# Performance work log

Hardware: AMD Instinct MI355X
Metric: run time of the kernel (lower is better)

The kernel has to match this reference:

```python
import jax, jax.numpy as jnp
import numpy as np

# normalization module stand-ins (simple monotone scalings, as in the repo they
# are fixed elementwise rescalings of the raw quantities)
def norm_local_x(n):
    return n

def norm_unit_contraction(c):
    return c

def norm_local_N(N):
    return jnp.log1p(N.astype(jnp.float32))

norm_TNG_radii = norm_local_x
norm_local_v = norm_local_x
norm_local_v0 = norm_local_x

EPS = 1e-5


def setup_inputs() -> dict:
    key = jax.random.key(0)
    ks = jax.random.split(key, 12)
    B, T, ND, KB = 2, 1024, 256, 3
    K_IN, H, L = 19, 128, 128
    x0 = 0.3 * jax.random.normal(ks[0], (B, T, 3), dtype=jnp.float32)
    # DM positions in local frame, |x| must stay < 1.05 (assert in original)
    x = jax.random.uniform(ks[1], (B, T, ND, 3), dtype=jnp.float32) - 0.5
    N = jax.random.randint(ks[2], (B, T), 1, 512, dtype=jnp.int32)
    basis = jax.random.normal(ks[3], (B, KB, 3), dtype=jnp.float32)
    v = jax.random.normal(ks[4], (B, T, ND, 3), dtype=jnp.float32)
    P200c = 0.5 + jax.random.uniform(ks[5], (B,), dtype=jnp.float32)
    s = 0.1
    W0 = s * jax.random.normal(ks[6], (K_IN, H - 1), dtype=jnp.float32)
    b0 = jnp.zeros((H - 1,), jnp.float32)
    W1 = s * jax.random.normal(ks[7], (H, H), dtype=jnp.float32)
    b1 = jnp.zeros((H,), jnp.float32)
    W2 = s * jax.random.normal(ks[8], (H, L), dtype=jnp.float32)
    b2 = jnp.zeros((L,), jnp.float32)
    return {"x0": x0, "x": x, "N": N, "basis": basis, "v": v, "P200c": P200c,
            "W0": W0, "b0": b0, "W1": W1, "b1": b1, "W2": W2, "b2": b2}


def create_scalars(x0, x, N, basis, v):
    B, T, ND, _ = x.shape
    # velocities relative to local mean (halo -> local frame)
    v0 = jnp.mean(v, axis=2)                      # [B,T,3]
    vc = v - v0[:, :, None, :]                    # [B,T,ND,3]

    x_norm = jnp.linalg.norm(x, axis=-1, keepdims=True) + EPS     # [B,T,ND,1]
    xu = x / x_norm
    x0_norm = jnp.linalg.norm(x0, axis=-1, keepdims=True) + EPS   # [B,T,1]
    x0u = x0 / x0_norm
    v0_norm = jnp.linalg.norm(v0, axis=-1, keepdims=True) + EPS   # [B,T,1]
    v0u = v0 / v0_norm
    v_norm = jnp.linalg.norm(vc, axis=-1, keepdims=True) + EPS    # [B,T,ND,1]
    vu = vc / v_norm

    bc = lambda a: jnp.broadcast_to(a[:, :, None, :], (B, T, ND, a.shape[-1]))

    feats = [
        norm_local_x(x_norm),                                          # |x| [1]
        norm_unit_contraction(jnp.einsum('btnd,bkd->btnk', xu, basis)),# x.basis [3]
        jnp.broadcast_to(norm_local_N(N)[:, :, None, None], (B, T, ND, 1)),  # N [1]
        bc(norm_TNG_radii(x0_norm)),                                   # |x0| [1]
        bc(norm_unit_contraction(jnp.einsum('btd,bkd->btk', x0u, basis))),  # x0.basis [3]
        bc(norm_local_v0(v0_norm)),                                    # |v0| [1]
        bc(norm_unit_contraction(jnp.einsum('btd,bkd->btk', v0u, basis))),  # v0.basis [3]
        bc(norm_unit_contraction(jnp.sum(x0u * v0u, axis=-1, keepdims=True))),  # x0.v0 [1]
        norm_local_v(v_norm),                                          # |v| [1]
        norm_unit_contraction(jnp.einsum('btnd,bkd->btnk', vu, basis)),# v.basis [3]
        norm_unit_contraction(jnp.sum(xu * vu, axis=-1, keepdims=True)),  # x.v [1]
    ]
    return jnp.concatenate(feats, axis=-1)  # [B,T,ND,19]


def reference(x0, x, N, basis, v, P200c, W0, b0, W1, b1, W2, b2):
    scalars = create_scalars(x0, x, N, basis, v)          # [B,T,ND,19]
    h = jax.nn.leaky_relu(scalars @ W0 + b0)              # [B,T,ND,H-1]
    h = jnp.mean(h, axis=2)                               # pool -> [B,T,H-1]
    h = jnp.concatenate([h, norm_local_N(N)[..., None]], axis=-1)  # [B,T,H]
    h = jax.nn.leaky_relu(h @ W1 + b1)                    # [B,T,H]
    out = h @ W2 + b2                                     # [B,T,Nlatent]
    return (1.0 / P200c)[:, None, None] * out
```

## Files before the change

### kernel.cpp

```cpp
#include <hip/hip_runtime.h>
#include <hip/hip_bf16.h>
#include <math.h>

#define EPSV 1e-5f
#define HD   128
#define WROW 40

typedef __attribute__((ext_vector_type(8))) short bf16x8;
typedef __attribute__((ext_vector_type(4))) float f32x4;

static __device__ __forceinline__ unsigned int bfbits(float x) {
    __hip_bfloat16 h = __float2bfloat16(x);
    unsigned short u;
    __builtin_memcpy(&u, &h, 2);
    return (unsigned int)u;
}

__global__ __launch_bounds__(256, 4) void net_fused(
    const float* __restrict__ x0g, const float* __restrict__ xg,
    const int*   __restrict__ Ng,  const float* __restrict__ basisg,
    const float* __restrict__ vg,  const float* __restrict__ Pg,
    const float* __restrict__ W0,  const float* __restrict__ b0,
    const float* __restrict__ W1,  const float* __restrict__ b1,
    const float* __restrict__ W2,  const float* __restrict__ b2,
    float* __restrict__ out, int Tn, int NDn)
{
    __shared__ __align__(16) __hip_bfloat16 Wt[128 * WROW];
    __shared__ float cvec[HD];
    __shared__ float hvec[HD];
    __shared__ float h1vec[HD];
    __shared__ float vred[4][3];

    const int bt   = blockIdx.x;
    const int b    = bt / Tn;
    const int tid  = threadIdx.x;
    const int lane = tid & 63;
    const int wave = tid >> 6;
    const int quad = lane >> 4;
    const int lm   = lane & 15;

    const long pbase = ((long)bt * NDn + tid) * 3;
    const float xi0 = xg[pbase+0], xi1 = xg[pbase+1], xi2 = xg[pbase+2];
    const float vi0 = vg[pbase+0], vi1 = vg[pbase+1], vi2 = vg[pbase+2];

    float s0 = vi0, s1 = vi1, s2 = vi2;
    #pragma unroll
    for (int off = 32; off > 0; off >>= 1) {
        s0 += __shfl_down(s0, off);
        s1 += __shfl_down(s1, off);
        s2 += __shfl_down(s2, off);
    }
    if (lane == 0) { vred[wave][0] = s0; vred[wave][1] = s1; vred[wave][2] = s2; }

    if (tid < 128) {
        const int RV[9] = {0, 1, 2, 3, 14, 15, 16, 17, 18};
        __hip_bfloat16 r1[32];
        #pragma unroll
        for (int kk = 0; kk < 32; ++kk) r1[kk] = __float2bfloat16(0.0f);
        if (tid < 127) {
            #pragma unroll
            for (int kk = 0; kk < 9; ++kk) {
                const float wv = W0[RV[kk] * 127 + tid];
                const __hip_bfloat16 hi = __float2bfloat16(wv);
                r1[kk]      = hi;
                r1[16 + kk] = __float2bfloat16(wv - __bfloat162float(hi));
            }
        }
        bf16x8* d1 = reinterpret_cast<bf16x8*>(&Wt[tid * WROW]);
        const bf16x8* s1v = reinterpret_cast<const bf16x8*>(r1);
        d1[0] = s1v[0]; d1[1] = s1v[1]; d1[2] = s1v[2]; d1[3] = s1v[3];
    }
    __syncthreads();

    const float inv_nd = 1.0f / (float)NDn;
    const float v00 = (vred[0][0]+vred[1][0]+vred[2][0]+vred[3][0]) * inv_nd;
    const float v01 = (vred[0][1]+vred[1][1]+vred[2][1]+vred[3][1]) * inv_nd;
    const float v02 = (vred[0][2]+vred[1][2]+vred[2][2]+vred[3][2]) * inv_nd;

    const float p0 = x0g[bt*3+0], p1 = x0g[bt*3+1], p2 = x0g[bt*3+2];
    float bas[3][3];
    #pragma unroll
    for (int k = 0; k < 3; ++k)
        #pragma unroll
        for (int c = 0; c < 3; ++c)
            bas[k][c] = basisg[(b*3 + k)*3 + c];

    const float x0n  = sqrtf(p0*p0 + p1*p1 + p2*p2) + EPSV;
    const float ix0n = 1.0f / x0n;
    const float x0u0 = p0*ix0n, x0u1 = p1*ix0n, x0u2 = p2*ix0n;

    const float v0n  = sqrtf(v00*v00 + v01*v01 + v02*v02) + EPSV;
    const float iv0n = 1.0f / v0n;
    const float v0u0 = v00*iv0n, v0u1 = v01*iv0n, v0u2 = v02*iv0n;

    const float logN = log1pf((float)Ng[bt]);

    if (tid < 128) {
        float c = 0.0f;
        if (tid < 127) {
            float fc[10];
            fc[0] = logN;
            fc[1] = x0n;
            fc[2] = x0u0*bas[0][0] + x0u1*bas[0][1] + x0u2*bas[0][2];
            fc[3] = x0u0*bas[1][0] + x0u1*bas[1][1] + x0u2*bas[1][2];
            fc[4] = x0u0*bas[2][0] + x0u1*bas[2][1] + x0u2*bas[2][2];
            fc[5] = v0n;
            fc[6] = v0u0*bas[0][0] + v0u1*bas[0][1] + v0u2*bas[0][2];
            fc[7] = v0u0*bas[1][0] + v0u1*bas[1][1] + v0u2*bas[1][2];
            fc[8] = v0u0*bas[2][0] + v0u1*bas[2][1] + v0u2*bas[2][2];
            fc[9] = x0u0*v0u0 + x0u1*v0u1 + x0u2*v0u2;
            c = b0[tid];
            #pragma unroll
            for (int i = 0; i < 10; ++i)
                c = fmaf(fc[i], W0[(4 + i) * 127 + tid], c);
        }
        cvec[tid] = c;
        hvec[tid] = (tid == 127) ? logN : 0.0f;
    }

    unsigned int H[5];
    {
        const float xn  = sqrtf(xi0*xi0 + xi1*xi1 + xi2*xi2) + EPSV;
        const float ixn = 1.0f / xn;
        const float xu0 = xi0*ixn, xu1 = xi1*ixn, xu2 = xi2*ixn;

        const float c0 = vi0 - v00, c1 = vi1 - v01, c2 = vi2 - v02;
        const float vn  = sqrtf(c0*c0 + c1*c1 + c2*c2) + EPSV;
        const float ivn = 1.0f / vn;
        const float vu0 = c0*ivn, vu1 = c1*ivn, vu2 = c2*ivn;

        float f[9];
        f[0] = xn;
        f[1] = xu0*bas[0][0] + xu1*bas[0][1] + xu2*bas[0][2];
        f[2] = xu0*bas[1][0] + xu1*bas[1][1] + xu2*bas[1][2];
        f[3] = xu0*bas[2][0] + xu1*bas[2][1] + xu2*bas[2][2];
        f[4] = vn;
        f[5] = vu0*bas[0][0] + vu1*bas[0][1] + vu2*bas[0][2];
        f[6] = vu0*bas[1][0] + vu1*bas[1][1] + vu2*bas[1][2];
        f[7] = vu0*bas[2][0] + vu1*bas[2][1] + vu2*bas[2][2];
        f[8] = xu0*vu0 + xu1*vu1 + xu2*vu2;

        unsigned int hb[9];
        #pragma unroll
        for (int kk = 0; kk < 9; ++kk) hb[kk] = bfbits(f[kk]);
        #pragma unroll
        for (int j = 0; j < 4; ++j) H[j] = hb[2*j] | (hb[2*j+1] << 16);
        H[4] = hb[8];
    }
    __syncthreads();

    {
        float pooled[8];
        #pragma unroll
        for (int nt = 0; nt < 8; ++nt) pooled[nt] = 0.0f;

        #pragma unroll
        for (int mt = 0; mt < 4; ++mt) {
            const int src = mt*16 + lm;
            const unsigned int t0 = (unsigned int)__shfl((int)H[0], src);
            const unsigned int t1 = (unsigned int)__shfl((int)H[1], src);
            const unsigned int t2 = (unsigned int)__shfl((int)H[2], src);
            const unsigned int t3 = (unsigned int)__shfl((int)H[3], src);
            const unsigned int t4 = (unsigned int)__shfl((int)H[4], src);

            union { unsigned int u[4]; bf16x8 v; } a;
            const bool evenq = ((quad & 1) == 0);
            a.u[0] = evenq ? t0 : t4;
            a.u[1] = evenq ? t1 : 0u;
            a.u[2] = evenq ? t2 : 0u;
            a.u[3] = evenq ? t3 : 0u;
            const bf16x8 af = a.v;

            #pragma unroll
            for (int nt = 0; nt < 8; ++nt) {
                const bf16x8 bf = *reinterpret_cast<const bf16x8*>(
                    &Wt[(nt*16 + lm) * WROW + quad*8]);
                const float cl = cvec[nt*16 + lm];
                const f32x4 cin = {cl, cl, cl, cl};
                const f32x4 acc = __builtin_amdgcn_mfma_f32_16x16x32_bf16(af, bf, cin, 0, 0, 0);
                #pragma unroll
                for (int r = 0; r < 4; ++r)
                    pooled[nt] += fmaxf(acc[r], 0.01f*acc[r]);
            }
        }
        #pragma unroll
        for (int nt = 0; nt < 8; ++nt) {
            pooled[nt] += __shfl_xor(pooled[nt], 16);
            pooled[nt] += __shfl_xor(pooled[nt], 32);
        }
        if (lane < 16) {
            #pragma unroll
            for (int nt = 0; nt < 8; ++nt) {
                atomicAdd(&hvec[nt*16 + lane], pooled[nt] * inv_nd);
            }
        }
    }
    __syncthreads();

    if (tid < HD) {
        float a = b1[tid];
        #pragma unroll 16
        for (int k = 0; k < HD; ++k)
            a = fmaf(hvec[k], W1[k*HD + tid], a);
        h1vec[tid] = fmaxf(a, 0.01f*a);
    }
    __syncthreads();

    if (tid < HD) {
        float a = b2[tid];
        #pragma unroll 16
        for (int k = 0; k < HD; ++k)
            a = fmaf(h1vec[k], W2[k*HD + tid], a);
        out[(long)bt * HD + tid] = a / Pg[b];
    }
}

extern "C" void kernel_launch(void* const* d_in, const int* in_sizes, int n_in,
                              void* d_out, int out_size, void* d_ws, size_t ws_size,
                              hipStream_t stream) {
    const float* x0    = (const float*)d_in[0];
    const float* x     = (const float*)d_in[1];
    const int*   N     = (const int*)  d_in[2];
    const float* basis = (const float*)d_in[3];
    const float* v     = (const float*)d_in[4];
    const float* P200c = (const float*)d_in[5];
    const float* W0    = (const float*)d_in[6];
    const float* b0    = (const float*)d_in[7];
    const float* W1    = (const float*)d_in[8];
    const float* b1    = (const float*)d_in[9];
    const float* W2    = (const float*)d_in[10];
    const float* b2    = (const float*)d_in[11];
    float* out = (float*)d_out;

    const int B  = in_sizes[5];
    const int T  = in_sizes[2] / B;
    const int ND = in_sizes[1] / (in_sizes[2] * 3);

    hipLaunchKernelGGL(net_fused, dim3(B * T), dim3(256), 0, stream,
                       x0, x, N, basis, v, P200c, W0, b0, W1, b1, W2, b2,
                       out, T, ND);
}
```

Before: 110.2 us.

## Process two (b,t) rows per block to amortize weight staging and MLP loads

Each block now handles two halo rows instead of one. The bf16 W0 staging into LDS is shared between them, and the W1/W2 weight reads in the tail MLP serve both rows at once. This halves the grid to 1024 blocks and cuts redundant per-block setup and global weight traffic. In exchange it raises register pressure and per-block serial work, and with half as many blocks it may reduce parallelism across the CUs.

```diff
diff --git a/kernel.cpp b/kernel.cpp
--- a/kernel.cpp
+++ b/kernel.cpp
@@ -23,34 +23,43 @@
     const float* __restrict__ W0,  const float* __restrict__ b0,
     const float* __restrict__ W1,  const float* __restrict__ b1,
     const float* __restrict__ W2,  const float* __restrict__ b2,
-    float* __restrict__ out, int Tn, int NDn)
+    float* __restrict__ out, int Tn, int NDn, int nbt)
 {
     __shared__ __align__(16) __hip_bfloat16 Wt[128 * WROW];
-    __shared__ float cvec[HD];
-    __shared__ float hvec[HD];
-    __shared__ float h1vec[HD];
-    __shared__ float vred[4][3];
-
-    const int bt   = blockIdx.x;
-    const int b    = bt / Tn;
+    __shared__ float cvec[2][HD];
+    __shared__ float hvec[2][HD];
+    __shared__ float h1vec[2][HD];
+    __shared__ float vred[2][4][3];
+
+    const int bt0 = blockIdx.x * 2;
+    int bt1g = bt0 + 1; if (bt1g >= nbt) bt1g = bt0;
+    const int bts[2] = { bt0, bt1g };
+
     const int tid  = threadIdx.x;
     const int lane = tid & 63;
     const int wave = tid >> 6;
     const int quad = lane >> 4;
     const int lm   = lane & 15;
 
-    const long pbase = ((long)bt * NDn + tid) * 3;
-    const float xi0 = xg[pbase+0], xi1 = xg[pbase+1], xi2 = xg[pbase+2];
-    const float vi0 = vg[pbase+0], vi1 = vg[pbase+1], vi2 = vg[pbase+2];
-
-    float s0 = vi0, s1 = vi1, s2 = vi2;
-    #pragma unroll
-    for (int off = 32; off > 0; off >>= 1) {
-        s0 += __shfl_down(s0, off);
-        s1 += __shfl_down(s1, off);
-        s2 += __shfl_down(s2, off);
-    }
-    if (lane == 0) { vred[wave][0] = s0; vred[wave][1] = s1; vred[wave][2] = s2; }
+    float xi[2][3], vi[2][3];
+    #pragma unroll
+    for (int t = 0; t < 2; ++t) {
+        const long pbase = ((long)bts[t] * NDn + tid) * 3;
+        xi[t][0] = xg[pbase+0]; xi[t][1] = xg[pbase+1]; xi[t][2] = xg[pbase+2];
+        vi[t][0] = vg[pbase+0]; vi[t][1] = vg[pbase+1]; vi[t][2] = vg[pbase+2];
+    }
+
+    #pragma unroll
+    for (int t = 0; t < 2; ++t) {
+        float s0 = vi[t][0], s1 = vi[t][1], s2 = vi[t][2];
+        #pragma unroll
+        for (int off = 32; off > 0; off >>= 1) {
+            s0 += __shfl_down(s0, off);
+            s1 += __shfl_down(s1, off);
+            s2 += __shfl_down(s2, off);
+        }
+        if (lane == 0) { vred[t][wave][0] = s0; vred[t][wave][1] = s1; vred[t][wave][2] = s2; }
+    }
 
     if (tid < 128) {
         const int RV[9] = {0, 1, 2, 3, 14, 15, 16, 17, 18};
@@ -73,83 +82,91 @@
     __syncthreads();
 
     const float inv_nd = 1.0f / (float)NDn;
-    const float v00 = (vred[0][0]+vred[1][0]+vred[2][0]+vred[3][0]) * inv_nd;
-    const float v01 = (vred[0][1]+vred[1][1]+vred[2][1]+vred[3][1]) * inv_nd;
-    const float v02 = (vred[0][2]+vred[1][2]+vred[2][2]+vred[3][2]) * inv_nd;
-
-    const float p0 = x0g[bt*3+0], p1 = x0g[bt*3+1], p2 = x0g[bt*3+2];
-    float bas[3][3];
-    #pragma unroll
-    for (int k = 0; k < 3; ++k)
-        #pragma unroll
-        for (int c = 0; c < 3; ++c)
-            bas[k][c] = basisg[(b*3 + k)*3 + c];
-
-    const float x0n  = sqrtf(p0*p0 + p1*p1 + p2*p2) + EPSV;
-    const float ix0n = 1.0f / x0n;
-    const float x0u0 = p0*ix0n, x0u1 = p1*ix0n, x0u2 = p2*ix0n;
-
-    const float v0n  = sqrtf(v00*v00 + v01*v01 + v02*v02) + EPSV;
-    const float iv0n = 1.0f / v0n;
-    const float v0u0 = v00*iv0n, v0u1 = v01*iv0n, v0u2 = v02*iv0n;
-
-    const float logN = log1pf((float)Ng[bt]);
-
-    if (tid < 128) {
-        float c = 0.0f;
-        if (tid < 127) {
-            float fc[10];
-            fc[0] = logN;
-            fc[1] = x0n;
-            fc[2] = x0u0*bas[0][0] + x0u1*bas[0][1] + x0u2*bas[0][2];
-            fc[3] = x0u0*bas[1][0] + x0u1*bas[1][1] + x0u2*bas[1][2];
-            fc[4] = x0u0*bas[2][0] + x0u1*bas[2][1] + x0u2*bas[2][2];
-            fc[5] = v0n;
-            fc[6] = v0u0*bas[0][0] + v0u1*bas[0][1] + v0u2*bas[0][2];
-            fc[7] = v0u0*bas[1][0] + v0u1*bas[1][1] + v0u2*bas[1][2];
-            fc[8] = v0u0*bas[2][0] + v0u1*bas[2][1] + v0u2*bas[2][2];
-            fc[9] = x0u0*v0u0 + x0u1*v0u1 + x0u2*v0u2;
-            c = b0[tid];
-            #pragma unroll
-            for (int i = 0; i < 10; ++i)
-                c = fmaf(fc[i], W0[(4 + i) * 127 + tid], c);
-        }
-        cvec[tid] = c;
-        hvec[tid] = (tid == 127) ? logN : 0.0f;
-    }
-
-    unsigned int H[5];
-    {
-        const float xn  = sqrtf(xi0*xi0 + xi1*xi1 + xi2*xi2) + EPSV;
-        const float ixn = 1.0f / xn;
-        const float xu0 = xi0*ixn, xu1 = xi1*ixn, xu2 = xi2*ixn;
-
-        const float c0 = vi0 - v00, c1 = vi1 - v01, c2 = vi2 - v02;
-        const float vn  = sqrtf(c0*c0 + c1*c1 + c2*c2) + EPSV;
-        const float ivn = 1.0f / vn;
-        const float vu0 = c0*ivn, vu1 = c1*ivn, vu2 = c2*ivn;
-
-        float f[9];
-        f[0] = xn;
-        f[1] = xu0*bas[0][0] + xu1*bas[0][1] + xu2*bas[0][2];
-        f[2] = xu0*bas[1][0] + xu1*bas[1][1] + xu2*bas[1][2];
-        f[3] = xu0*bas[2][0] + xu1*bas[2][1] + xu2*bas[2][2];
-        f[4] = vn;
-        f[5] = vu0*bas[0][0] + vu1*bas[0][1] + vu2*bas[0][2];
-        f[6] = vu0*bas[1][0] + vu1*bas[1][1] + vu2*bas[1][2];
-        f[7] = vu0*bas[2][0] + vu1*bas[2][1] + vu2*bas[2][2];
-        f[8] = xu0*vu0 + xu1*vu1 + xu2*vu2;
-
-        unsigned int hb[9];
-        #pragma unroll
-        for (int kk = 0; kk < 9; ++kk) hb[kk] = bfbits(f[kk]);
-        #pragma unroll
-        for (int j = 0; j < 4; ++j) H[j] = hb[2*j] | (hb[2*j+1] << 16);
-        H[4] = hb[8];
-    }
-    __syncthreads();
-
-    {
+
+    unsigned int Hf[2][5];
+    #pragma unroll
+    for (int t = 0; t < 2; ++t) {
+        const int bt = bts[t];
+        const int b  = bt / Tn;
+
+        const float v00 = (vred[t][0][0]+vred[t][1][0]+vred[t][2][0]+vred[t][3][0]) * inv_nd;
+        const float v01 = (vred[t][0][1]+vred[t][1][1]+vred[t][2][1]+vred[t][3][1]) * inv_nd;
+        const float v02 = (vred[t][0][2]+vred[t][1][2]+vred[t][2][2]+vred[t][3][2]) * inv_nd;
+
+        const float p0 = x0g[bt*3+0], p1 = x0g[bt*3+1], p2 = x0g[bt*3+2];
+        float bas[3][3];
+        #pragma unroll
+        for (int k = 0; k < 3; ++k)
+            #pragma unroll
+            for (int c = 0; c < 3; ++c)
+                bas[k][c] = basisg[(b*3 + k)*3 + c];
+
+        const float x0n  = sqrtf(p0*p0 + p1*p1 + p2*p2) + EPSV;
+        const float ix0n = 1.0f / x0n;
+        const float x0u0 = p0*ix0n, x0u1 = p1*ix0n, x0u2 = p2*ix0n;
+
+        const float v0n  = sqrtf(v00*v00 + v01*v01 + v02*v02) + EPSV;
+        const float iv0n = 1.0f / v0n;
+        const float v0u0 = v00*iv0n, v0u1 = v01*iv0n, v0u2 = v02*iv0n;
+
+        const float logN = log1pf((float)Ng[bt]);
+
+        if (tid < 128) {
+            float c = 0.0f;
+            if (tid < 127) {
+                float fc[10];
+                fc[0] = logN;
+                fc[1] = x0n;
+                fc[2] = x0u0*bas[0][0] + x0u1*bas[0][1] + x0u2*bas[0][2];
+                fc[3] = x0u0*bas[1][0] + x0u1*bas[1][1] + x0u2*bas[1][2];
+                fc[4] = x0u0*bas[2][0] + x0u1*bas[2][1] + x0u2*bas[2][2];
+                fc[5] = v0n;
+                fc[6] = v0u0*bas[0][0] + v0u1*bas[0][1] + v0u2*bas[0][2];
+                fc[7] = v0u0*bas[1][0] + v0u1*bas[1][1] + v0u2*bas[1][2];
+                fc[8] = v0u0*bas[2][0] + v0u1*bas[2][1] + v0u2*bas[2][2];
+                fc[9] = x0u0*v0u0 + x0u1*v0u1 + x0u2*v0u2;
+                c = b0[tid];
+                #pragma unroll
+                for (int i = 0; i < 10; ++i)
+                    c = fmaf(fc[i], W0[(4 + i) * 127 + tid], c);
+            }
+            cvec[t][tid] = c;
+            hvec[t][tid] = (tid == 127) ? logN : 0.0f;
+        }
+
+        {
+            const float xn  = sqrtf(xi[t][0]*xi[t][0] + xi[t][1]*xi[t][1] + xi[t][2]*xi[t][2]) + EPSV;
+            const float ixn = 1.0f / xn;
+            const float xu0 = xi[t][0]*ixn, xu1 = xi[t][1]*ixn, xu2 = xi[t][2]*ixn;
+
+            const float c0 = vi[t][0] - v00, c1 = vi[t][1] - v01, c2 = vi[t][2] - v02;
+            const float vn  = sqrtf(c0*c0 + c1*c1 + c2*c2) + EPSV;
+            const float ivn = 1.0f / vn;
+            const float vu0 = c0*ivn, vu1 = c1*ivn, vu2 = c2*ivn;
+
+            float f[9];
+            f[0] = xn;
+            f[1] = xu0*bas[0][0] + xu1*bas[0][1] + xu2*bas[0][2];
+            f[2] = xu0*bas[1][0] + xu1*bas[1][1] + xu2*bas[1][2];
+            f[3] = xu0*bas[2][0] + xu1*bas[2][1] + xu2*bas[2][2];
+            f[4] = vn;
+            f[5] = vu0*bas[0][0] + vu1*bas[0][1] + vu2*bas[0][2];
+            f[6] = vu0*bas[1][0] + vu1*bas[1][1] + vu2*bas[1][2];
+            f[7] = vu0*bas[2][0] + vu1*bas[2][1] + vu2*bas[2][2];
+            f[8] = xu0*vu0 + xu1*vu1 + xu2*vu2;
+
+            unsigned int hb[9];
+            #pragma unroll
+            for (int kk = 0; kk < 9; ++kk) hb[kk] = bfbits(f[kk]);
+            #pragma unroll
+            for (int j = 0; j < 4; ++j) Hf[t][j] = hb[2*j] | (hb[2*j+1] << 16);
+            Hf[t][4] = hb[8];
+        }
+    }
+    __syncthreads();
+
+    #pragma unroll
+    for (int t = 0; t < 2; ++t) {
         float pooled[8];
         #pragma unroll
         for (int nt = 0; nt < 8; ++nt) pooled[nt] = 0.0f;
@@ -157,11 +174,11 @@
         #pragma unroll
         for (int mt = 0; mt < 4; ++mt) {
             const int src = mt*16 + lm;
-            const unsigned int t0 = (unsigned int)__shfl((int)H[0], src);
-            const unsigned int t1 = (unsigned int)__shfl((int)H[1], src);
-            const unsigned int t2 = (unsigned int)__shfl((int)H[2], src);
-            const unsigned int t3 = (unsigned int)__shfl((int)H[3], src);
-            const unsigned int t4 = (unsigned int)__shfl((int)H[4], src);
+            const unsigned int t0 = (unsigned int)__shfl((int)Hf[t][0], src);
+            const unsigned int t1 = (unsigned int)__shfl((int)Hf[t][1], src);
+            const unsigned int t2 = (unsigned int)__shfl((int)Hf[t][2], src);
+            const unsigned int t3 = (unsigned int)__shfl((int)Hf[t][3], src);
+            const unsigned int t4 = (unsigned int)__shfl((int)Hf[t][4], src);
 
             union { unsigned int u[4]; bf16x8 v; } a;
             const bool evenq = ((quad & 1) == 0);
@@ -175,7 +192,7 @@
             for (int nt = 0; nt < 8; ++nt) {
                 const bf16x8 bf = *reinterpret_cast<const bf16x8*>(
                     &Wt[(nt*16 + lm) * WROW + quad*8]);
-                const float cl = cvec[nt*16 + lm];
+                const float cl = cvec[t][nt*16 + lm];
                 const f32x4 cin = {cl, cl, cl, cl};
                 const f32x4 acc = __builtin_amdgcn_mfma_f32_16x16x32_bf16(af, bf, cin, 0, 0, 0);
                 #pragma unroll
@@ -191,27 +208,35 @@
         if (lane < 16) {
             #pragma unroll
             for (int nt = 0; nt < 8; ++nt) {
-                atomicAdd(&hvec[nt*16 + lane], pooled[nt] * inv_nd);
+                atomicAdd(&hvec[t][nt*16 + lane], pooled[nt] * inv_nd);
             }
         }
     }
     __syncthreads();
 
     if (tid < HD) {
-        float a = b1[tid];
-        #pragma unroll 16
-        for (int k = 0; k < HD; ++k)
-            a = fmaf(hvec[k], W1[k*HD + tid], a);
-        h1vec[tid] = fmaxf(a, 0.01f*a);
+        float a0 = b1[tid], a1 = a0;
+        #pragma unroll 8
+        for (int k = 0; k < HD; ++k) {
+            const float w = W1[k*HD + tid];
+            a0 = fmaf(hvec[0][k], w, a0);
+            a1 = fmaf(hvec[1][k], w, a1);
+        }
+        h1vec[0][tid] = fmaxf(a0, 0.01f*a0);
+        h1vec[1][tid] = fmaxf(a1, 0.01f*a1);
     }
     __syncthreads();
 
     if (tid < HD) {
-        float a = b2[tid];
-        #pragma unroll 16
-        for (int k = 0; k < HD; ++k)
-            a = fmaf(h1vec[k], W2[k*HD + tid], a);
-        out[(long)bt * HD + tid] = a / Pg[b];
+        float a0 = b2[tid], a1 = a0;
+        #pragma unroll 8
+        for (int k = 0; k < HD; ++k) {
+            const float w = W2[k*HD + tid];
+            a0 = fmaf(h1vec[0][k], w, a0);
+            a1 = fmaf(h1vec[1][k], w, a1);
+        }
+        out[(long)bts[0] * HD + tid] = a0 / Pg[bts[0] / Tn];
+        out[(long)bts[1] * HD + tid] = a1 / Pg[bts[1] / Tn];
     }
 }
 
@@ -235,8 +260,9 @@
     const int B  = in_sizes[5];
     const int T  = in_sizes[2] / B;
     const int ND = in_sizes[1] / (in_sizes[2] * 3);
-
-    hipLaunchKernelGGL(net_fused, dim3(B * T), dim3(256), 0, stream,
+    const int nbt = B * T;
+
+    hipLaunchKernelGGL(net_fused, dim3((nbt + 1) / 2), dim3(256), 0, stream,
                        x0, x, N, basis, v, P200c, W0, b0, W1, b1, W2, b2,
-                       out, T, ND);
+                       out, T, ND, nbt);
 }
```

After: 108.1 us. Within noise of the previous version (-1.9%).
